# Kernel optimization log

Hardware: AMD Instinct MI355X
Metric: run time of the kernel (lower is better)

Reference implementation:

```python
import jax, jax.numpy as jnp
import numpy as np

ALPHA = 2.0   # surrogate.atan(alpha=2)
BETA = 0.9    # membrane decay
THR = 1.0     # spike threshold

@jax.custom_vjp
def atan_spike(x):
    # Heaviside forward, atan surrogate backward (snntorch convention)
    return (x > 0).astype(x.dtype)

def _atan_fwd(x):
    return atan_spike(x), x

def _atan_bwd(x, g):
    return (g * (ALPHA / 2.0) / (1.0 + (jnp.pi / 2.0 * ALPHA * x) ** 2),)

atan_spike.defvjp(_atan_fwd, _atan_bwd)


def setup_inputs() -> dict:
    key = jax.random.key(0)
    ks = jax.random.split(key, 7)
    B, T, I = 128, 128, 1024
    dims = [2048, 2048, 1024]
    x = jax.random.normal(ks[0], (B, T, I), dtype=jnp.float32)
    fan_ins = [I, dims[0], dims[1]]
    W0 = jax.random.normal(ks[1], (dims[0], fan_ins[0]), dtype=jnp.float32) / np.sqrt(fan_ins[0])
    b0 = jax.random.normal(ks[2], (dims[0],), dtype=jnp.float32) * 0.01
    W1 = jax.random.normal(ks[3], (dims[1], fan_ins[1]), dtype=jnp.float32) / np.sqrt(fan_ins[1])
    b1 = jax.random.normal(ks[4], (dims[1],), dtype=jnp.float32) * 0.01
    W2 = jax.random.normal(ks[5], (dims[2], fan_ins[2]), dtype=jnp.float32) / np.sqrt(fan_ins[2])
    b2 = jax.random.normal(ks[6], (dims[2],), dtype=jnp.float32) * 0.01
    return {"x": x, "W0": W0, "b0": b0, "W1": W1, "b1": b1, "W2": W2, "b2": b2}


def reference(x, W0, b0, W1, b1, W2, b2):
    params = ((W0, b0), (W1, b1), (W2, b2))
    B = x.shape[0]
    dims = [W0.shape[0], W1.shape[0], W2.shape[0]]
    v0 = tuple(jnp.zeros((B, d), x.dtype) for d in dims)

    def step(volts, x_t):
        h = x_t
        new_volts = []
        v = None
        for (W, b), vi in zip(params, volts):
            cur = h @ W.T + b            # [B, d]
            v = BETA * vi + cur           # leaky integration
            spk = atan_spike(v - THR)     # threshold
            v = v - spk * THR             # reset by subtraction
            new_volts.append(v)
            h = spk
        return tuple(new_volts), (h, v)

    xT = jnp.swapaxes(x, 0, 1)            # [T, B, I]
    _, (spikes, volts) = jax.lax.scan(step, v0, xT)
    # [T, B, D] -> [B, T, D]
    return jnp.swapaxes(spikes, 0, 1), jnp.swapaxes(volts, 0, 1)
```

## Files before the change

kernel.cpp:

```cpp
#include <hip/hip_runtime.h>
#include <stdint.h>


#define TT   128
#define NB   128
#define DD2  1024

#define SPK0_OFF 0u
#define SPK1_OFF (128u*128u*64u)
#define PART_OFF (2u*128u*128u*64u)
#define NHELP    192u
#define FLG_OFF  (PART_OFF + NHELP*4096u)
#define NFLG     1536u
#define WS_NEED_BYTES ((size_t)(FLG_OFF + NFLG) * 4u)

__device__ __forceinline__ void wait_ge(uint32_t* p, uint32_t tgt){
  while (__hip_atomic_load(p, __ATOMIC_ACQUIRE, __HIP_MEMORY_SCOPE_AGENT) < tgt)
    __builtin_amdgcn_s_sleep(1);
}

__device__ __forceinline__ constexpr int fswz(int k){
  return (k & 16) | ((k ^ (k >> 3)) & 12);
}

__global__ void sentinel_kernel(float* o){ o[0] = 42.0f; }

__global__ __launch_bounds__(512, 2) void snn_kernel(
    const float* __restrict__ x,
    const float* __restrict__ W0, const float* __restrict__ b0,
    const float* __restrict__ W1, const float* __restrict__ b1,
    const float* __restrict__ W2, const float* __restrict__ b2,
    float* __restrict__ out, uint32_t* __restrict__ ws)
{
  __shared__ __align__(16) float lA[2][128][68];
  __shared__ __align__(16) float lB[2][32][132];
  __shared__ uint32_t lBits2[2][64];

  const int tid  = threadIdx.x;
  const int h    = tid >> 8;
  const int t256 = tid & 255;
  const int tm   = t256 & 15;
  const int tn   = t256 >> 4;
  const int bid  = blockIdx.x;

  uint32_t* spikes0 = ws + SPK0_OFF;
  uint32_t* spikes1 = ws + SPK1_OFF;
  uint32_t* flg   = ws + FLG_OFF;
  uint32_t* done0 = flg + 1024;
  uint32_t* done1 = flg + 1280;

  int group, tl, m0, n0, K, K0, dTgt;
  const float *Wl, *bl;
  const uint32_t* spkIn; uint32_t* spkOut;
  uint32_t *dIn, *dOut;
  if (bid < 64) {
    group=0; tl=bid*2+h;
    m0=(tl>>6)*64; n0=(tl&63)*32; K=1024; K0=0; Wl=W0; bl=b0;
    spkIn=nullptr; spkOut=spikes0; dIn=nullptr; dOut=done0+(m0>>6)*128; dTgt=0;
  } else if (bid < 192) {
    group=1; tl=bid-64;
    m0=(tl>>6)*64; n0=(tl&63)*32; K=2048; K0=h*1024; Wl=W1; bl=b1;
    spkIn=spikes0; spkOut=spikes1;
    dIn=done0+(m0>>6)*128; dOut=done1+(m0>>6)*128; dTgt=32;
  } else {
    group=2; tl=bid-192;
    m0=(tl>>5)*64; n0=(tl&31)*32; K=2048; K0=h*1024; Wl=W2; bl=b2;
    spkIn=spikes1; spkOut=nullptr;
    dIn=done1+(m0>>6)*128; dOut=nullptr; dTgt=64;
  }
  const bool own = (group == 0) || (h == 0);

  const float bias0 = bl[n0 + tn*2 + 0];
  const float bias1 = bl[n0 + tn*2 + 1];

  float vst[4][2];
  #pragma unroll
  for (int r = 0; r < 4; ++r) { vst[r][0] = 0.f; vst[r][1] = 0.f; }

  const int e_mq   = t256 & 15;
  const int e_sub  = t256 >> 4;
  const int e_wsub = e_sub & 3;
  const int e_kq8  = e_sub >> 2;
  const int e_kloc = e_wsub*32 + e_kq8*8;

  float (*cA)[68]  = lA[h];
  float (*cB)[132] = lB[h];

  for (int t = 0; t < TT; ++t) {
    if (dIn) {
      if (tid == 0) wait_ge(&dIn[t], (uint32_t)dTgt);
      __syncthreads();
    }

    float acc2[2][4][2];
    #pragma unroll
    for (int p = 0; p < 2; ++p)
      #pragma unroll
      for (int r = 0; r < 4; ++r) { acc2[p][r][0] = 0.f; acc2[p][r][1] = 0.f; }

    #pragma unroll
    for (int p = 0; p < 2; ++p) {
      #pragma unroll 1
      for (int ch = 0; ch < 4; ++ch) {
        const int kb = K0 + p*512 + ch*128;

        #pragma unroll
        for (int it = 0; it < 4; ++it) {
          int idx = t256 + it*256;
          int nrow = idx >> 5, kq = idx & 31;
          float4 w = *(const float4*)(Wl + (size_t)(n0+nrow)*K + kb + kq*4);
          *(float4*)&cB[nrow][kq*4] = w;
        }

        if (group == 0) {
          #pragma unroll
          for (int it = 0; it < 8; ++it) {
            int idx = t256 + it*256;
            int mrow = idx >> 5, kq = idx & 31;
            float4 v = *(const float4*)(x + ((size_t)(m0+mrow)*TT + t)*1024 + kb + kq*4);
            int k0 = kq*4;
            lA[h][k0+0][mrow ^ fswz(k0+0)] = v.x;
            lA[h][k0+1][mrow ^ fswz(k0+1)] = v.y;
            lA[h][k0+2][mrow ^ fswz(k0+2)] = v.z;
            lA[h][k0+3][mrow ^ fswz(k0+3)] = v.w;
          }
        } else {
          const size_t rbase = ((size_t)t*NB + m0 + e_mq*4)*64 + (kb>>5) + e_wsub;
          uint32_t w0 = __hip_atomic_load(&spkIn[rbase      ], __ATOMIC_RELAXED, __HIP_MEMORY_SCOPE_AGENT);
          uint32_t w1 = __hip_atomic_load(&spkIn[rbase +  64], __ATOMIC_RELAXED, __HIP_MEMORY_SCOPE_AGENT);
          uint32_t w2 = __hip_atomic_load(&spkIn[rbase + 128], __ATOMIC_RELAXED, __HIP_MEMORY_SCOPE_AGENT);
          uint32_t w3 = __hip_atomic_load(&spkIn[rbase + 192], __ATOMIC_RELAXED, __HIP_MEMORY_SCOPE_AGENT);
          #pragma unroll
          for (int i = 0; i < 8; ++i) {
            int k  = e_kloc + i;
            int sh = k & 31;
            float4 f;
            f.x = ((w0 >> sh) & 1u) ? 1.0f : 0.0f;
            f.y = ((w1 >> sh) & 1u) ? 1.0f : 0.0f;
            f.z = ((w2 >> sh) & 1u) ? 1.0f : 0.0f;
            f.w = ((w3 >> sh) & 1u) ? 1.0f : 0.0f;
            *(float4*)&cA[k][(e_mq*4) ^ fswz(k)] = f;
          }
        }
        __syncthreads();

        #pragma unroll 4
        for (int k4 = 0; k4 < 32; ++k4) {
          const int kbase = k4*4;
          const int sw = fswz(kbase);
          const float* pa = &cA[kbase][(tm*4) ^ sw];
          const float4 b0v = *(const float4*)&cB[tn*2    ][kbase];
          const float4 b1v = *(const float4*)&cB[tn*2 + 1][kbase];
          #pragma unroll
          for (int u = 0; u < 4; ++u) {
            const float4 a  = *(const float4*)(pa + u*68);
            const float bv0 = (u==0) ? b0v.x : (u==1) ? b0v.y : (u==2) ? b0v.z : b0v.w;
            const float bv1 = (u==0) ? b1v.x : (u==1) ? b1v.y : (u==2) ? b1v.z : b1v.w;
            acc2[p][0][0] = __builtin_fmaf(a.x, bv0, acc2[p][0][0]);
            acc2[p][1][0] = __builtin_fmaf(a.y, bv0, acc2[p][1][0]);
            acc2[p][2][0] = __builtin_fmaf(a.z, bv0, acc2[p][2][0]);
            acc2[p][3][0] = __builtin_fmaf(a.w, bv0, acc2[p][3][0]);
            acc2[p][0][1] = __builtin_fmaf(a.x, bv1, acc2[p][0][1]);
            acc2[p][1][1] = __builtin_fmaf(a.y, bv1, acc2[p][1][1]);
            acc2[p][2][1] = __builtin_fmaf(a.z, bv1, acc2[p][2][1]);
            acc2[p][3][1] = __builtin_fmaf(a.w, bv1, acc2[p][3][1]);
          }
        }
        __syncthreads();
      }
    }

    float acc[4][2];
    #pragma unroll
    for (int r = 0; r < 4; ++r) {
      acc[r][0] = __fadd_rn(acc2[0][r][0], acc2[1][r][0]);
      acc[r][1] = __fadd_rn(acc2[0][r][1], acc2[1][r][1]);
    }

    if (group != 0) {
      float* ex = &lA[1][0][0];
      if (h == 1) {
        #pragma unroll
        for (int q = 0; q < 4; ++q) {
          const int hh = q >> 1, rb = (q & 1) * 2;
          *(float4*)&ex[t256*16 + q*4] = make_float4(
              acc2[hh][rb+0][0], acc2[hh][rb+0][1],
              acc2[hh][rb+1][0], acc2[hh][rb+1][1]);
        }
      }
      __syncthreads();
      if (h == 0) {
        #pragma unroll
        for (int hh = 0; hh < 2; ++hh)
          #pragma unroll
          for (int r = 0; r < 4; ++r) {
            acc[r][0] = __fadd_rn(acc[r][0], ex[t256*16 + hh*8 + r*2 + 0]);
            acc[r][1] = __fadd_rn(acc[r][1], ex[t256*16 + hh*8 + r*2 + 1]);
          }
      }
    }

    if (group < 2) { if (t256 < 64) lBits2[h][t256] = 0; __syncthreads(); }

    if (own) {
      float sv[4][2], vv8[4][2];
      #pragma unroll
      for (int r = 0; r < 4; ++r) {
        uint32_t msk = 0;
        #pragma unroll
        for (int c = 0; c < 2; ++c) {
          float cur = __fadd_rn(acc[r][c], c ? bias1 : bias0);
          float vv  = __fadd_rn(__fmul_rn(0.9f, vst[r][c]), cur);
          float s   = (vv > 1.0f) ? 1.0f : 0.0f;
          vv = __fsub_rn(vv, s);
          vst[r][c] = vv;
          sv[r][c] = s; vv8[r][c] = vv;
          msk |= (s != 0.f) ? (1u << (tn*2 + c)) : 0u;
        }
        if (group < 2 && msk) atomicOr(&lBits2[h][tm*4 + r], msk);
      }
      if (group == 2) {
        #pragma unroll
        for (int r = 0; r < 4; ++r) {
          size_t o  = ((size_t)(m0 + tm*4 + r)*TT + t)*DD2 + n0 + tn*2;
          *(float2*)(out + o)  = make_float2(sv[r][0], sv[r][1]);
          size_t ov = (size_t)NB*TT*DD2 + o;
          *(float2*)(out + ov) = make_float2(vv8[r][0], vv8[r][1]);
        }
      }
    }

    if (group < 2) {
      __syncthreads();
      if (own && t256 < 64)
        __hip_atomic_store(&spkOut[((size_t)t*NB + m0 + t256)*64 + (n0>>5)],
                           lBits2[h][t256], __ATOMIC_RELAXED, __HIP_MEMORY_SCOPE_AGENT);
      __syncthreads();
      if (tid == 0) __hip_atomic_fetch_add(&dOut[t], 1u, __ATOMIC_RELEASE, __HIP_MEMORY_SCOPE_AGENT);
    }
  }
}

extern "C" void kernel_launch(void* const* d_in, const int* in_sizes, int n_in,
                              void* d_out, int out_size, void* d_ws, size_t ws_size,
                              hipStream_t stream) {
  (void)in_sizes; (void)n_in; (void)out_size;
  float* outf = (float*)d_out;
  if (ws_size < WS_NEED_BYTES) {
    sentinel_kernel<<<1, 1, 0, stream>>>(outf);
    return;
  }
  const float* x  = (const float*)d_in[0];
  const float* W0 = (const float*)d_in[1];
  const float* b0 = (const float*)d_in[2];
  const float* W1 = (const float*)d_in[3];
  const float* b1 = (const float*)d_in[4];
  const float* W2 = (const float*)d_in[5];
  const float* b2 = (const float*)d_in[6];
  uint32_t* ws = (uint32_t*)d_ws;

  hipMemsetAsync(ws + FLG_OFF, 0, NFLG * sizeof(uint32_t), stream);

  snn_kernel<<<256, 512, 0, stream>>>(x, W0, b0, W1, b1, W2, b2, outf, ws);
}
```

Measured before the change: 7.061 ms.

## Widen N tiles to 64 and split K across helper/owner block pairs

```diff
diff --git a/kernel.cpp b/kernel.cpp
--- a/kernel.cpp
+++ b/kernel.cpp
@@ -9,8 +9,8 @@
 #define SPK0_OFF 0u
 #define SPK1_OFF (128u*128u*64u)
 #define PART_OFF (2u*128u*128u*64u)
-#define NHELP    192u
-#define FLG_OFF  (PART_OFF + NHELP*4096u)
+#define NHELP    96u
+#define FLG_OFF  (PART_OFF + NHELP*8192u)
 #define NFLG     1536u
 #define WS_NEED_BYTES ((size_t)(FLG_OFF + NFLG) * 4u)
 
@@ -33,8 +33,8 @@
     float* __restrict__ out, uint32_t* __restrict__ ws)
 {
   __shared__ __align__(16) float lA[2][128][68];
-  __shared__ __align__(16) float lB[2][32][132];
-  __shared__ uint32_t lBits2[2][64];
+  __shared__ __align__(16) float lB[2][64][132];
+  __shared__ uint32_t lBits[128];
 
   const int tid  = threadIdx.x;
   const int h    = tid >> 8;
@@ -43,39 +43,46 @@
   const int tn   = t256 >> 4;
   const int bid  = blockIdx.x;
 
-  uint32_t* spikes0 = ws + SPK0_OFF;
-  uint32_t* spikes1 = ws + SPK1_OFF;
+  uint32_t* spikes0  = ws + SPK0_OFF;
+  uint32_t* spikes1  = ws + SPK1_OFF;
+  float*    partials = (float*)(ws + PART_OFF);
   uint32_t* flg   = ws + FLG_OFF;
+  uint32_t* pflag = flg;
+  uint32_t* oflag = flg + 512;
   uint32_t* done0 = flg + 1024;
   uint32_t* done1 = flg + 1280;
 
-  int group, tl, m0, n0, K, K0, dTgt;
+  int group, pairk, tl, m0, n0, K, hslot;
   const float *Wl, *bl;
   const uint32_t* spkIn; uint32_t* spkOut;
   uint32_t *dIn, *dOut;
   if (bid < 64) {
-    group=0; tl=bid*2+h;
-    m0=(tl>>6)*64; n0=(tl&63)*32; K=1024; K0=0; Wl=W0; bl=b0;
-    spkIn=nullptr; spkOut=spikes0; dIn=nullptr; dOut=done0+(m0>>6)*128; dTgt=0;
+    group=0; pairk=0; tl=bid;
+    m0=(tl>>5)*64; n0=(tl&31)*64; K=1024; Wl=W0; bl=b0;
+    spkIn=nullptr; spkOut=spikes0; dIn=nullptr; dOut=done0+(m0>>6)*128; hslot=-1;
   } else if (bid < 192) {
-    group=1; tl=bid-64;
-    m0=(tl>>6)*64; n0=(tl&63)*32; K=2048; K0=h*1024; Wl=W1; bl=b1;
+    group=1; int rel=bid-64; pairk=rel&1; tl=rel>>1;
+    m0=(tl>>5)*64; n0=(tl&31)*64; K=2048; Wl=W1; bl=b1;
     spkIn=spikes0; spkOut=spikes1;
-    dIn=done0+(m0>>6)*128; dOut=done1+(m0>>6)*128; dTgt=32;
+    dIn=done0+(m0>>6)*128; dOut=done1+(m0>>6)*128; hslot=tl;
   } else {
-    group=2; tl=bid-192;
-    m0=(tl>>5)*64; n0=(tl&31)*32; K=2048; K0=h*1024; Wl=W2; bl=b2;
+    group=2; int rel=bid-192; pairk=rel&1; tl=rel>>1;
+    m0=(tl>>4)*64; n0=(tl&15)*64; K=2048; Wl=W2; bl=b2;
     spkIn=spikes1; spkOut=nullptr;
-    dIn=done1+(m0>>6)*128; dOut=nullptr; dTgt=64;
+    dIn=done1+(m0>>6)*128; dOut=nullptr; hslot=64+tl;
   }
-  const bool own = (group == 0) || (h == 0);
-
-  const float bias0 = bl[n0 + tn*2 + 0];
-  const float bias1 = bl[n0 + tn*2 + 1];
-
-  float vst[4][2];
+  const bool helper = (pairk == 1);
+  const int  K0     = (pairk*2 + h)*512;
+
+  float bias[4];
   #pragma unroll
-  for (int r = 0; r < 4; ++r) { vst[r][0] = 0.f; vst[r][1] = 0.f; }
+  for (int c = 0; c < 4; ++c) bias[c] = bl[n0 + tn*4 + c];
+
+  float vst[4][4];
+  #pragma unroll
+  for (int r = 0; r < 4; ++r)
+    #pragma unroll
+    for (int c = 0; c < 4; ++c) vst[r][c] = 0.f;
 
   const int e_mq   = t256 & 15;
   const int e_sub  = t256 >> 4;
@@ -85,156 +92,196 @@
 
   float (*cA)[68]  = lA[h];
   float (*cB)[132] = lB[h];
+  float* ex = &lA[1][0][0];
 
   for (int t = 0; t < TT; ++t) {
     if (dIn) {
-      if (tid == 0) wait_ge(&dIn[t], (uint32_t)dTgt);
-      __syncthreads();
-    }
-
-    float acc2[2][4][2];
+      if (tid == 0) wait_ge(&dIn[t], 32u);
+      __syncthreads();
+    }
+
+    float acc[4][4];
     #pragma unroll
-    for (int p = 0; p < 2; ++p)
-      #pragma unroll
-      for (int r = 0; r < 4; ++r) { acc2[p][r][0] = 0.f; acc2[p][r][1] = 0.f; }
-
-    #pragma unroll
-    for (int p = 0; p < 2; ++p) {
-      #pragma unroll 1
-      for (int ch = 0; ch < 4; ++ch) {
-        const int kb = K0 + p*512 + ch*128;
-
-        #pragma unroll
-        for (int it = 0; it < 4; ++it) {
+    for (int r = 0; r < 4; ++r)
+      #pragma unroll
+      for (int c = 0; c < 4; ++c) acc[r][c] = 0.f;
+
+    #pragma unroll 1
+    for (int ch = 0; ch < 4; ++ch) {
+      const int kb = K0 + ch*128;
+
+      #pragma unroll
+      for (int it = 0; it < 8; ++it) {
+        int idx = t256 + it*256;
+        int nrow = idx >> 5, kq = idx & 31;
+        float4 w = *(const float4*)(Wl + (size_t)(n0+nrow)*K + kb + kq*4);
+        *(float4*)&cB[nrow][kq*4] = w;
+      }
+
+      if (group == 0) {
+        #pragma unroll
+        for (int it = 0; it < 8; ++it) {
           int idx = t256 + it*256;
-          int nrow = idx >> 5, kq = idx & 31;
-          float4 w = *(const float4*)(Wl + (size_t)(n0+nrow)*K + kb + kq*4);
-          *(float4*)&cB[nrow][kq*4] = w;
-        }
-
-        if (group == 0) {
+          int mrow = idx >> 5, kq = idx & 31;
+          float4 v = *(const float4*)(x + ((size_t)(m0+mrow)*TT + t)*1024 + kb + kq*4);
+          int k0 = kq*4;
+          const int sw = fswz(k0);
+          const int col = mrow ^ sw;
+          cA[k0+0][col] = v.x; cA[k0+1][col] = v.y;
+          cA[k0+2][col] = v.z; cA[k0+3][col] = v.w;
+        }
+      } else {
+        const size_t rbase = ((size_t)t*NB + m0 + e_mq*4)*64 + (kb>>5) + e_wsub;
+        uint32_t w0 = __hip_atomic_load(&spkIn[rbase      ], __ATOMIC_RELAXED, __HIP_MEMORY_SCOPE_AGENT);
+        uint32_t w1 = __hip_atomic_load(&spkIn[rbase +  64], __ATOMIC_RELAXED, __HIP_MEMORY_SCOPE_AGENT);
+        uint32_t w2 = __hip_atomic_load(&spkIn[rbase + 128], __ATOMIC_RELAXED, __HIP_MEMORY_SCOPE_AGENT);
+        uint32_t w3 = __hip_atomic_load(&spkIn[rbase + 192], __ATOMIC_RELAXED, __HIP_MEMORY_SCOPE_AGENT);
+        #pragma unroll
+        for (int i = 0; i < 8; ++i) {
+          int k  = e_kloc + i;
+          int sh = k & 31;
+          float4 f;
+          f.x = ((w0 >> sh) & 1u) ? 1.0f : 0.0f;
+          f.y = ((w1 >> sh) & 1u) ? 1.0f : 0.0f;
+          f.z = ((w2 >> sh) & 1u) ? 1.0f : 0.0f;
+          f.w = ((w3 >> sh) & 1u) ? 1.0f : 0.0f;
+          *(float4*)&cA[k][(e_mq*4) ^ fswz(k)] = f;
+        }
+      }
+      __syncthreads();
+
+      #pragma unroll 4
+      for (int k4 = 0; k4 < 32; ++k4) {
+        const int kbase = k4*4;
+        const int sw = fswz(kbase);
+        const float* pa = &cA[kbase][(tm*4) ^ sw];
+        const float4 q0 = *(const float4*)&cB[tn*4+0][kbase];
+        const float4 q1 = *(const float4*)&cB[tn*4+1][kbase];
+        const float4 q2 = *(const float4*)&cB[tn*4+2][kbase];
+        const float4 q3 = *(const float4*)&cB[tn*4+3][kbase];
+        #pragma unroll
+        for (int u = 0; u < 4; ++u) {
+          const float4 a  = *(const float4*)(pa + u*68);
+          const float b0v = (u==0) ? q0.x : (u==1) ? q0.y : (u==2) ? q0.z : q0.w;
+          const float b1v = (u==0) ? q1.x : (u==1) ? q1.y : (u==2) ? q1.z : q1.w;
+          const float b2v = (u==0) ? q2.x : (u==1) ? q2.y : (u==2) ? q2.z : q2.w;
+          const float b3v = (u==0) ? q3.x : (u==1) ? q3.y : (u==2) ? q3.z : q3.w;
+          acc[0][0] = __builtin_fmaf(a.x, b0v, acc[0][0]);
+          acc[1][0] = __builtin_fmaf(a.y, b0v, acc[1][0]);
+          acc[2][0] = __builtin_fmaf(a.z, b0v, acc[2][0]);
+          acc[3][0] = __builtin_fmaf(a.w, b0v, acc[3][0]);
+          acc[0][1] = __builtin_fmaf(a.x, b1v, acc[0][1]);
+          acc[1][1] = __builtin_fmaf(a.y, b1v, acc[1][1]);
+          acc[2][1] = __builtin_fmaf(a.z, b1v, acc[2][1]);
+          acc[3][1] = __builtin_fmaf(a.w, b1v, acc[3][1]);
+          acc[0][2] = __builtin_fmaf(a.x, b2v, acc[0][2]);
+          acc[1][2] = __builtin_fmaf(a.y, b2v, acc[1][2]);
+          acc[2][2] = __builtin_fmaf(a.z, b2v, acc[2][2]);
+          acc[3][2] = __builtin_fmaf(a.w, b2v, acc[3][2]);
+          acc[0][3] = __builtin_fmaf(a.x, b3v, acc[0][3]);
+          acc[1][3] = __builtin_fmaf(a.y, b3v, acc[1][3]);
+          acc[2][3] = __builtin_fmaf(a.z, b3v, acc[2][3]);
+          acc[3][3] = __builtin_fmaf(a.w, b3v, acc[3][3]);
+        }
+      }
+      __syncthreads();
+    }
+
+    if (helper) {
+      if (t >= 1) { if (tid == 0) wait_ge(&oflag[bid-1], (uint32_t)t); __syncthreads(); }
+      uint64_t* pb = (uint64_t*)(partials + (size_t)hslot*8192 + (size_t)h*4096) + t256*8;
+      #pragma unroll
+      for (int r = 0; r < 4; ++r)
+        #pragma unroll
+        for (int cq = 0; cq < 2; ++cq) {
+          union { float f[2]; uint64_t u; } cv;
+          cv.f[0] = acc[r][cq*2+0]; cv.f[1] = acc[r][cq*2+1];
+          __hip_atomic_store(&pb[r*2+cq], cv.u, __ATOMIC_RELAXED, __HIP_MEMORY_SCOPE_AGENT);
+        }
+      __syncthreads();
+      if (tid == 0) __hip_atomic_store(&pflag[bid], (uint32_t)(t+1), __ATOMIC_RELEASE, __HIP_MEMORY_SCOPE_AGENT);
+      continue;
+    }
+
+    if (h == 1) {
+      #pragma unroll
+      for (int r = 0; r < 4; ++r)
+        *(float4*)&ex[t256*16 + r*4] = make_float4(acc[r][0], acc[r][1], acc[r][2], acc[r][3]);
+    }
+    __syncthreads();
+    if (h == 0) {
+      #pragma unroll
+      for (int r = 0; r < 4; ++r)
+        #pragma unroll
+        for (int c = 0; c < 4; ++c)
+          acc[r][c] = __fadd_rn(acc[r][c], ex[t256*16 + r*4 + c]);
+    }
+
+    if (group != 0) {
+      if (tid == 0) wait_ge(&pflag[bid+1], (uint32_t)(t+1));
+      __syncthreads();
+      if (h == 0) {
+        uint64_t* p2 = (uint64_t*)(partials + (size_t)hslot*8192) + t256*8;
+        uint64_t* p3 = (uint64_t*)(partials + (size_t)hslot*8192 + 4096) + t256*8;
+        #pragma unroll
+        for (int r = 0; r < 4; ++r)
           #pragma unroll
-          for (int it = 0; it < 8; ++it) {
-            int idx = t256 + it*256;
-            int mrow = idx >> 5, kq = idx & 31;
-            float4 v = *(const float4*)(x + ((size_t)(m0+mrow)*TT + t)*1024 + kb + kq*4);
-            int k0 = kq*4;
-            lA[h][k0+0][mrow ^ fswz(k0+0)] = v.x;
-            lA[h][k0+1][mrow ^ fswz(k0+1)] = v.y;
-            lA[h][k0+2][mrow ^ fswz(k0+2)] = v.z;
-            lA[h][k0+3][mrow ^ fswz(k0+3)] = v.w;
+          for (int cq = 0; cq < 2; ++cq) {
+            union { uint64_t u; float f[2]; } cv;
+            cv.u = __hip_atomic_load(&p2[r*2+cq], __ATOMIC_RELAXED, __HIP_MEMORY_SCOPE_AGENT);
+            acc[r][cq*2+0] = __fadd_rn(acc[r][cq*2+0], cv.f[0]);
+            acc[r][cq*2+1] = __fadd_rn(acc[r][cq*2+1], cv.f[1]);
           }
-        } else {
-          const size_t rbase = ((size_t)t*NB + m0 + e_mq*4)*64 + (kb>>5) + e_wsub;
-          uint32_t w0 = __hip_atomic_load(&spkIn[rbase      ], __ATOMIC_RELAXED, __HIP_MEMORY_SCOPE_AGENT);
-          uint32_t w1 = __hip_atomic_load(&spkIn[rbase +  64], __ATOMIC_RELAXED, __HIP_MEMORY_SCOPE_AGENT);
-          uint32_t w2 = __hip_atomic_load(&spkIn[rbase + 128], __ATOMIC_RELAXED, __HIP_MEMORY_SCOPE_AGENT);
-          uint32_t w3 = __hip_atomic_load(&spkIn[rbase + 192], __ATOMIC_RELAXED, __HIP_MEMORY_SCOPE_AGENT);
+        #pragma unroll
+        for (int r = 0; r < 4; ++r)
           #pragma unroll
-          for (int i = 0; i < 8; ++i) {
-            int k  = e_kloc + i;
-            int sh = k & 31;
-            float4 f;
-            f.x = ((w0 >> sh) & 1u) ? 1.0f : 0.0f;
-            f.y = ((w1 >> sh) & 1u) ? 1.0f : 0.0f;
-            f.z = ((w2 >> sh) & 1u) ? 1.0f : 0.0f;
-            f.w = ((w3 >> sh) & 1u) ? 1.0f : 0.0f;
-            *(float4*)&cA[k][(e_mq*4) ^ fswz(k)] = f;
+          for (int cq = 0; cq < 2; ++cq) {
+            union { uint64_t u; float f[2]; } cv;
+            cv.u = __hip_atomic_load(&p3[r*2+cq], __ATOMIC_RELAXED, __HIP_MEMORY_SCOPE_AGENT);
+            acc[r][cq*2+0] = __fadd_rn(acc[r][cq*2+0], cv.f[0]);
+            acc[r][cq*2+1] = __fadd_rn(acc[r][cq*2+1], cv.f[1]);
           }
-        }
-        __syncthreads();
-
-        #pragma unroll 4
-        for (int k4 = 0; k4 < 32; ++k4) {
-          const int kbase = k4*4;
-          const int sw = fswz(kbase);
-          const float* pa = &cA[kbase][(tm*4) ^ sw];
-          const float4 b0v = *(const float4*)&cB[tn*2    ][kbase];
-          const float4 b1v = *(const float4*)&cB[tn*2 + 1][kbase];
-          #pragma unroll
-          for (int u = 0; u < 4; ++u) {
-            const float4 a  = *(const float4*)(pa + u*68);
-            const float bv0 = (u==0) ? b0v.x : (u==1) ? b0v.y : (u==2) ? b0v.z : b0v.w;
-            const float bv1 = (u==0) ? b1v.x : (u==1) ? b1v.y : (u==2) ? b1v.z : b1v.w;
-            acc2[p][0][0] = __builtin_fmaf(a.x, bv0, acc2[p][0][0]);
-            acc2[p][1][0] = __builtin_fmaf(a.y, bv0, acc2[p][1][0]);
-            acc2[p][2][0] = __builtin_fmaf(a.z, bv0, acc2[p][2][0]);
-            acc2[p][3][0] = __builtin_fmaf(a.w, bv0, acc2[p][3][0]);
-            acc2[p][0][1] = __builtin_fmaf(a.x, bv1, acc2[p][0][1]);
-            acc2[p][1][1] = __builtin_fmaf(a.y, bv1, acc2[p][1][1]);
-            acc2[p][2][1] = __builtin_fmaf(a.z, bv1, acc2[p][2][1]);
-            acc2[p][3][1] = __builtin_fmaf(a.w, bv1, acc2[p][3][1]);
-          }
-        }
-        __syncthreads();
-      }
-    }
-
-    float acc[4][2];
-    #pragma unroll
-    for (int r = 0; r < 4; ++r) {
-      acc[r][0] = __fadd_rn(acc2[0][r][0], acc2[1][r][0]);
-      acc[r][1] = __fadd_rn(acc2[0][r][1], acc2[1][r][1]);
-    }
-
-    if (group != 0) {
-      float* ex = &lA[1][0][0];
-      if (h == 1) {
-        #pragma unroll
-        for (int q = 0; q < 4; ++q) {
-          const int hh = q >> 1, rb = (q & 1) * 2;
-          *(float4*)&ex[t256*16 + q*4] = make_float4(
-              acc2[hh][rb+0][0], acc2[hh][rb+0][1],
-              acc2[hh][rb+1][0], acc2[hh][rb+1][1]);
-        }
-      }
-      __syncthreads();
-      if (h == 0) {
-        #pragma unroll
-        for (int hh = 0; hh < 2; ++hh)
-          #pragma unroll
-          for (int r = 0; r < 4; ++r) {
-            acc[r][0] = __fadd_rn(acc[r][0], ex[t256*16 + hh*8 + r*2 + 0]);
-            acc[r][1] = __fadd_rn(acc[r][1], ex[t256*16 + hh*8 + r*2 + 1]);
-          }
-      }
-    }
-
-    if (group < 2) { if (t256 < 64) lBits2[h][t256] = 0; __syncthreads(); }
-
-    if (own) {
-      float sv[4][2], vv8[4][2];
+      }
+      __syncthreads();
+      if (tid == 0) __hip_atomic_store(&oflag[bid], (uint32_t)(t+1), __ATOMIC_RELEASE, __HIP_MEMORY_SCOPE_AGENT);
+    }
+
+    if (group < 2) { if (tid < 128) lBits[tid] = 0; __syncthreads(); }
+
+    if (h == 0) {
+      float sv[4][4], vv8[4][4];
       #pragma unroll
       for (int r = 0; r < 4; ++r) {
         uint32_t msk = 0;
         #pragma unroll
-        for (int c = 0; c < 2; ++c) {
-          float cur = __fadd_rn(acc[r][c], c ? bias1 : bias0);
+        for (int c = 0; c < 4; ++c) {
+          float cur = __fadd_rn(acc[r][c], bias[c]);
           float vv  = __fadd_rn(__fmul_rn(0.9f, vst[r][c]), cur);
           float s   = (vv > 1.0f) ? 1.0f : 0.0f;
           vv = __fsub_rn(vv, s);
           vst[r][c] = vv;
           sv[r][c] = s; vv8[r][c] = vv;
-          msk |= (s != 0.f) ? (1u << (tn*2 + c)) : 0u;
-        }
-        if (group < 2 && msk) atomicOr(&lBits2[h][tm*4 + r], msk);
+          msk |= (s != 0.f) ? (1u << c) : 0u;
+        }
+        if (group < 2 && msk)
+          atomicOr(&lBits[(tm*4 + r)*2 + (tn>>3)], msk << ((tn&7)*4));
       }
       if (group == 2) {
         #pragma unroll
         for (int r = 0; r < 4; ++r) {
-          size_t o  = ((size_t)(m0 + tm*4 + r)*TT + t)*DD2 + n0 + tn*2;
-          *(float2*)(out + o)  = make_float2(sv[r][0], sv[r][1]);
+          size_t o  = ((size_t)(m0 + tm*4 + r)*TT + t)*DD2 + n0 + tn*4;
+          *(float4*)(out + o)  = make_float4(sv[r][0], sv[r][1], sv[r][2], sv[r][3]);
           size_t ov = (size_t)NB*TT*DD2 + o;
-          *(float2*)(out + ov) = make_float2(vv8[r][0], vv8[r][1]);
+          *(float4*)(out + ov) = make_float4(vv8[r][0], vv8[r][1], vv8[r][2], vv8[r][3]);
         }
       }
     }
 
     if (group < 2) {
       __syncthreads();
-      if (own && t256 < 64)
-        __hip_atomic_store(&spkOut[((size_t)t*NB + m0 + t256)*64 + (n0>>5)],
-                           lBits2[h][t256], __ATOMIC_RELAXED, __HIP_MEMORY_SCOPE_AGENT);
+      if (tid < 128)
+        __hip_atomic_store(&spkOut[((size_t)t*NB + m0 + (tid>>1))*64 + (n0>>5) + (tid&1)],
+                           lBits[tid], __ATOMIC_RELAXED, __HIP_MEMORY_SCOPE_AGENT);
       __syncthreads();
       if (tid == 0) __hip_atomic_fetch_add(&dOut[t], 1u, __ATOMIC_RELEASE, __HIP_MEMORY_SCOPE_AGENT);
     }
```

Result: faster. 6.312 ms (-10.6%).
